# Performance work log

Measured on AMD Instinct MI355X. Metric: run time of the kernel, lower is better.

The kernel has to match this reference:

```python
import jax, jax.numpy as jnp
import numpy as np

HID = 1024
H = 8        # num_attention_heads
KV = 2       # num_key_value_heads
HD = HID // H  # head_dim = 128
G = H // KV    # kv groups = 4
EPS = 1e-6


def setup_inputs() -> dict:
    key = jax.random.key(0)
    ks = jax.random.split(key, 12)
    B, S = 4, 2048
    s = 0.02
    inp = {
        "hidden_states": jax.random.normal(ks[0], (B, S, HID), jnp.float32),
        "rope": jax.random.normal(ks[1], (1, 1, S, 2 * HD), jnp.float32),
        # q_proj outputs 2*H*HD (query + elementwise gate)
        "Wq": jax.random.normal(ks[2], (HID, 2 * H * HD), jnp.float32) * s,
        "bq": jnp.zeros((2 * H * HD,), jnp.float32),
        "Wk": jax.random.normal(ks[3], (HID, KV * HD), jnp.float32) * s,
        "bk": jnp.zeros((KV * HD,), jnp.float32),
        "Wv": jax.random.normal(ks[4], (HID, KV * HD), jnp.float32) * s,
        "bv": jnp.zeros((KV * HD,), jnp.float32),
        "Wo": jax.random.normal(ks[5], (H * HD, HID), jnp.float32) * s,
        "bo": jnp.zeros((HID,), jnp.float32),
        "q_norm_w": jnp.ones((HD,), jnp.float32),
        "k_norm_w": jnp.ones((HD,), jnp.float32),
    }
    return inp


def _rmsnorm(x, w):
    var = jnp.mean(jnp.square(x), axis=-1, keepdims=True)
    return x * jax.lax.rsqrt(var + EPS) * w


def _rot(x):
    # interleaved rotation: [-x1, x0, -x3, x2, ...]
    x2 = x.reshape(x.shape[:-1] + (HD // 2, 2))
    r = jnp.stack([-x2[..., 1], x2[..., 0]], axis=-1)
    return r.reshape(x.shape)


def _apply_rope_cat(x, emb):
    # emb: [S, 2*HD] = cat(sin, cos); x: [B, h, S, HD]
    sin, cos = jnp.split(emb, 2, axis=-1)
    sin = sin[None, None]
    cos = cos[None, None]
    return x * cos + _rot(x) * sin


def reference(hidden_states, rope, Wq, bq, Wk, bk, Wv, bv, Wo, bo, q_norm_w, k_norm_w):
    B, S, _ = hidden_states.shape
    qg = hidden_states @ Wq + bq                     # [B,S,2*H*HD]
    qg = qg.reshape(B, S, KV, -1)                    # [B,S,KV, 2*G*HD]
    q, gate = jnp.split(qg, [HD * G], axis=-1)       # [B,S,KV,G*HD], [B,S,KV,G*HD]
    gate = gate.reshape(B, S, H, HD)                 # [B,S,H,HD]
    q = q.reshape(B, S, H, HD).transpose(0, 2, 1, 3) # [B,H,S,HD]
    k = (hidden_states @ Wk + bk).reshape(B, S, KV, HD).transpose(0, 2, 1, 3)
    v = (hidden_states @ Wv + bv).reshape(B, S, KV, HD).transpose(0, 2, 1, 3)

    q = _rmsnorm(q, q_norm_w)
    k = _rmsnorm(k, k_norm_w)

    emb = rope[0, 0, :S]                             # [S, 2*HD]
    q = _apply_rope_cat(q, emb)
    k = _apply_rope_cat(k, emb)

    # GQA: repeat kv heads to match query heads
    k = jnp.repeat(k, G, axis=1)                     # [B,H,S,HD]
    v = jnp.repeat(v, G, axis=1)

    scale = 1.0 / jnp.sqrt(jnp.asarray(HD, q.dtype))
    scores = jnp.einsum("bhqd,bhkd->bhqk", q, k) * scale
    attn = jax.nn.softmax(scores, axis=-1)
    out = jnp.einsum("bhqk,bhkd->bhqd", attn, v)     # [B,H,S,HD]

    out = out.transpose(0, 2, 1, 3)                  # [B,S,H,HD]
    out = out * jax.nn.sigmoid(gate)
    out = out.reshape(B, S, H * HD)
    return out @ Wo + bo
```

## Files before the change

kernel.cpp:

```cpp
#include <hip/hip_runtime.h>
#include <math.h>

#define SCALE_ 0.08838834764831845f
#define PSHIFT 8.0f

typedef __attribute__((ext_vector_type(8))) short short8;
typedef __attribute__((ext_vector_type(4))) float floatx4;
typedef __attribute__((ext_vector_type(4))) _Float16 half4;

__device__ inline short f2bf(float x) {
    union { float f; unsigned u; } v; v.f = x;
    unsigned r = v.u + 0x7fff + ((v.u >> 16) & 1);
    return (short)(r >> 16);
}
__device__ inline float bf2f(short h) {
    union { float f; unsigned u; } v; v.u = ((unsigned)(unsigned short)h) << 16;
    return v.f;
}

__global__ __launch_bounds__(256) void convert_x(
    const float* __restrict__ X, short* __restrict__ Xb,
    const float* __restrict__ bq, const float* __restrict__ bk2,
    const float* __restrict__ bv2, float* __restrict__ bcat)
{
    const int gid = blockIdx.x * 256 + threadIdx.x;
    if (gid < 2097152) {
        const float4 v = ((const float4*)X)[gid];
        short4 o;
        o.x = f2bf(v.x); o.y = f2bf(v.y); o.z = f2bf(v.z); o.w = f2bf(v.w);
        ((short4*)Xb)[gid] = o;
    }
    if (gid < 2560)
        bcat[gid] = (gid < 2048) ? bq[gid]
                  : (gid < 2304) ? bk2[gid - 2048] : bv2[gid - 2304];
}

__global__ __launch_bounds__(256) void wtrans(
    const float* __restrict__ Wq, const float* __restrict__ Wk,
    const float* __restrict__ Wv, const float* __restrict__ Wo,
    short* __restrict__ Wt, short* __restrict__ Wot)
{
    __shared__ float T[32][33];
    const int t = threadIdx.x;
    const int k0 = blockIdx.x * 32;
    const int ny = blockIdx.y;
    const float* src; int ldn, ncol0, nrow0; short* dst;
    if (ny < 80) {
        const int n0 = ny * 32;
        if (n0 < 2048)      { src = Wq; ldn = 2048; ncol0 = n0; }
        else if (n0 < 2304) { src = Wk; ldn = 256;  ncol0 = n0 - 2048; }
        else                { src = Wv; ldn = 256;  ncol0 = n0 - 2304; }
        dst = Wt; nrow0 = n0;
    } else {
        const int n0 = (ny - 80) * 32;
        src = Wo; ldn = 1024; ncol0 = n0; dst = Wot; nrow0 = n0;
    }
    {
        const int r = t >> 3, c4 = (t & 7) * 4;
        const float4 v = *(const float4*)&src[(size_t)(k0 + r) * ldn + ncol0 + c4];
        T[r][c4 + 0] = v.x; T[r][c4 + 1] = v.y; T[r][c4 + 2] = v.z; T[r][c4 + 3] = v.w;
    }
    __syncthreads();
    {
        const int nr = t >> 3, kc4 = (t & 7) * 4;
        short4 o;
        o.x = f2bf(T[kc4 + 0][nr]);
        o.y = f2bf(T[kc4 + 1][nr]);
        o.z = f2bf(T[kc4 + 2][nr]);
        o.w = f2bf(T[kc4 + 3][nr]);
        *(short4*)&dst[(size_t)(nrow0 + nr) * 1024 + k0 + kc4] = o;
    }
}

__global__ __launch_bounds__(256) void qkv_mfma(
    const short* __restrict__ Ag, const short* __restrict__ Bg,
    const float* __restrict__ bcat,
    short* __restrict__ qb, short* __restrict__ kb,
    short* __restrict__ vb, short* __restrict__ gateb)
{
    __shared__ short As[128 * 64];
    __shared__ short Bs[128 * 64];
    const int tid = threadIdx.x;
    const int wave = tid >> 6, lane = tid & 63;
    const int quad = lane >> 4, l16 = lane & 15;
    const int wm = wave & 1, wn = wave >> 1;
    const int m0 = blockIdx.y * 128, n0 = blockIdx.x * 128;

    floatx4 acc[4][4] = {};

    for (int k0 = 0; k0 < 1024; k0 += 64) {
        __syncthreads();
        #pragma unroll
        for (int c = 0; c < 4; ++c) {
            const int blk = (c * 4 + wave) * 64 + lane;
            const int row = blk >> 3, p = blk & 7;
            const int col = (p ^ (row & 7)) << 3;
            __builtin_amdgcn_global_load_lds(
                (const __attribute__((address_space(1))) unsigned int*)(Ag + (size_t)(m0 + row) * 1024 + k0 + col),
                (__attribute__((address_space(3))) unsigned int*)&As[(c * 4 + wave) * 512],
                16, 0, 0);
            __builtin_amdgcn_global_load_lds(
                (const __attribute__((address_space(1))) unsigned int*)(Bg + (size_t)(n0 + row) * 1024 + k0 + col),
                (__attribute__((address_space(3))) unsigned int*)&Bs[(c * 4 + wave) * 512],
                16, 0, 0);
        }
        __syncthreads();
        #pragma unroll
        for (int ks = 0; ks < 2; ++ks) {
            short8 af[4], bfr[4];
            #pragma unroll
            for (int mt = 0; mt < 4; ++mt) {
                const int row = wm * 64 + mt * 16 + l16;
                const int p = (ks * 4 + quad) ^ (row & 7);
                af[mt] = *(const short8*)&As[row * 64 + p * 8];
            }
            #pragma unroll
            for (int nt = 0; nt < 4; ++nt) {
                const int row = wn * 64 + nt * 16 + l16;
                const int p = (ks * 4 + quad) ^ (row & 7);
                bfr[nt] = *(const short8*)&Bs[row * 64 + p * 8];
            }
            #pragma unroll
            for (int mt = 0; mt < 4; ++mt)
                #pragma unroll
                for (int nt = 0; nt < 4; ++nt)
                    acc[mt][nt] = __builtin_amdgcn_mfma_f32_16x16x32_bf16(af[mt], bfr[nt], acc[mt][nt], 0, 0, 0);
        }
    }

    #pragma unroll
    for (int nt = 0; nt < 4; ++nt) {
        const int n = n0 + wn * 64 + nt * 16 + l16;
        const float bias = bcat[n];
        #pragma unroll
        for (int mt = 0; mt < 4; ++mt) {
            #pragma unroll
            for (int r = 0; r < 4; ++r) {
                const int m = m0 + wm * 64 + mt * 16 + quad * 4 + r;
                const int b = m >> 11, s = m & 2047;
                const short o = f2bf(acc[mt][nt][r] + bias);
                if (n < 2048) {
                    const int kv = n >> 10, rr = n & 1023;
                    if (rr < 512) {
                        const int h = kv * 4 + (rr >> 7), d = rr & 127;
                        qb[(((size_t)(b * 8 + h)) * 2048 + s) * 128 + d] = o;
                    } else {
                        const int r2 = rr - 512;
                        const int h = kv * 4 + (r2 >> 7), d = r2 & 127;
                        gateb[(size_t)m * 1024 + h * 128 + d] = o;
                    }
                } else if (n < 2304) {
                    const int c = n - 2048;
                    kb[(((size_t)(b * 2 + (c >> 7))) * 2048 + s) * 128 + (c & 127)] = o;
                } else {
                    const int c = n - 2304;
                    vb[(((size_t)(b * 2 + (c >> 7))) * 2048 + s) * 128 + (c & 127)] = o;
                }
            }
        }
    }
}

__global__ __launch_bounds__(256) void norm_rope(
    short* __restrict__ qb, short* __restrict__ kb,
    const float* __restrict__ rope,
    const float* __restrict__ qw, const float* __restrict__ kw)
{
    const int row = blockIdx.x * 4 + (threadIdx.x >> 6);
    short* base; const float* w; int s; float scl;
    if (row < 65536) { base = qb + (size_t)row * 128; s = row & 2047; w = qw; scl = SCALE_; }
    else { const int r2 = row - 65536; base = kb + (size_t)r2 * 128; s = r2 & 2047; w = kw; scl = 1.0f; }
    const int lane = threadIdx.x & 63;
    const short2 xv = *(const short2*)&base[lane * 2];
    const float x0 = bf2f(xv.x), x1 = bf2f(xv.y);
    float ssq = x0 * x0 + x1 * x1;
    #pragma unroll
    for (int off = 1; off < 64; off <<= 1) ssq += __shfl_xor(ssq, off);
    const float inv = rsqrtf(ssq * (1.0f / 128.0f) + 1e-6f);
    const float a = x0 * inv * w[lane * 2];
    const float b = x1 * inv * w[lane * 2 + 1];
    const float* er = rope + (size_t)s * 256;
    const float sin0 = er[lane * 2], sin1 = er[lane * 2 + 1];
    const float cos0 = er[128 + lane * 2], cos1 = er[128 + lane * 2 + 1];
    short2 o;
    o.x = f2bf((a * cos0 - b * sin0) * scl);
    o.y = f2bf((b * cos1 + a * sin1) * scl);
    *(short2*)&base[lane * 2] = o;
}

__global__ __launch_bounds__(256) void vtrans(
    const short* __restrict__ vb, _Float16* __restrict__ vt)
{
    __shared__ float T[32][33];
    const int t = threadIdx.x;
    const int s0 = blockIdx.x * 32, d0 = blockIdx.y * 32, bk = blockIdx.z;
    const short* src = vb + ((size_t)bk * 2048 + s0) * 128 + d0;
    {
        const int sr = t >> 3, c4 = (t & 7) * 4;
        const short4 xv = *(const short4*)&src[sr * 128 + c4];
        T[sr][c4 + 0] = bf2f(xv.x);
        T[sr][c4 + 1] = bf2f(xv.y);
        T[sr][c4 + 2] = bf2f(xv.z);
        T[sr][c4 + 3] = bf2f(xv.w);
    }
    __syncthreads();
    {
        const int dr = t >> 3, sc4 = (t & 7) * 4;
        half4 o;
        o[0] = (_Float16)T[sc4 + 0][dr];
        o[1] = (_Float16)T[sc4 + 1][dr];
        o[2] = (_Float16)T[sc4 + 2][dr];
        o[3] = (_Float16)T[sc4 + 3][dr];
        *(half4*)&vt[((size_t)bk * 128 + d0 + dr) * 2048 + s0 + sc4] = o;
    }
}

__global__ __launch_bounds__(256) void attn_mfma(
    const short* __restrict__ qb, const short* __restrict__ kb,
    const _Float16* __restrict__ vt, const short* __restrict__ gateb,
    short* __restrict__ xo)
{
    __shared__ short   Ks[64][132];
    __shared__ _Float16 VTs[128][68];

    const int tid = threadIdx.x;
    const int wave = tid >> 6, lane = tid & 63;
    const int quad = lane >> 4, l16 = lane & 15;
    const int bh = blockIdx.y, b = bh >> 3, h = bh & 7, kv = h >> 2;
    const int q0 = blockIdx.x * 64;

    short8 qf[4];
    {
        const short* qbase = qb + (((size_t)(b * 8 + h)) * 2048 + q0 + wave * 16 + l16) * 128;
        #pragma unroll
        for (int ks = 0; ks < 4; ++ks)
            qf[ks] = *(const short8*)&qbase[ks * 32 + quad * 8];
    }

    const short*    kbase  = kb + (size_t)(b * 2 + kv) * 2048 * 128;
    const _Float16* vtbase = vt + (size_t)(b * 2 + kv) * 128 * 2048;

    floatx4 O[8] = {};
    float lsum = 0.0f;

    for (int kt = 0; kt < 32; ++kt) {
        __syncthreads();
        const short* kg = kbase + (size_t)kt * 64 * 128;
        #pragma unroll
        for (int i = 0; i < 4; ++i) {
            const int idx = tid + i * 256;
            const int r = idx >> 4, c = (idx & 15) * 8;
            *(short8*)&Ks[r][c] = *(const short8*)&kg[r * 128 + c];
        }
        const _Float16* vg = vtbase + kt * 64;
        #pragma unroll
        for (int i = 0; i < 4; ++i) {
            const int idx = tid + i * 256;
            const int r = idx >> 3, c = (idx & 7) * 8;
            *(float4*)&VTs[r][c] = *(const float4*)&vg[(size_t)r * 2048 + c];
        }
        __syncthreads();

        floatx4 ST[4];
        #pragma unroll
        for (int jt = 0; jt < 4; ++jt) {
            ST[jt] = (floatx4){0.f, 0.f, 0.f, 0.f};
            #pragma unroll
            for (int ks = 0; ks < 4; ++ks) {
                const short8 af = *(const short8*)&Ks[jt * 16 + l16][ks * 32 + quad * 8];
                ST[jt] = __builtin_amdgcn_mfma_f32_16x16x32_bf16(af, qf[ks], ST[jt], 0, 0, 0);
            }
        }

        half4 pf[4];
        #pragma unroll
        for (int jt = 0; jt < 4; ++jt) {
            const float p0 = __expf(ST[jt][0] - PSHIFT);
            const float p1 = __expf(ST[jt][1] - PSHIFT);
            const float p2 = __expf(ST[jt][2] - PSHIFT);
            const float p3 = __expf(ST[jt][3] - PSHIFT);
            lsum += (p0 + p1) + (p2 + p3);
            pf[jt][0] = (_Float16)p0;
            pf[jt][1] = (_Float16)p1;
            pf[jt][2] = (_Float16)p2;
            pf[jt][3] = (_Float16)p3;
        }

        #pragma unroll
        for (int jt = 0; jt < 4; ++jt) {
            #pragma unroll
            for (int dt = 0; dt < 8; ++dt) {
                const half4 va = *(const half4*)&VTs[dt * 16 + l16][jt * 16 + quad * 4];
                O[dt] = __builtin_amdgcn_mfma_f32_16x16x16f16(va, pf[jt], O[dt], 0, 0, 0);
            }
        }
    }

    {
        float ps = lsum;
        ps += __shfl_xor(ps, 16);
        ps += __shfl_xor(ps, 32);
        const float invl = 1.0f / ps;
        const int s = q0 + wave * 16 + l16;
        const size_t base = ((size_t)b * 2048 + s) * 1024 + h * 128;
        #pragma unroll
        for (int dt = 0; dt < 8; ++dt) {
            const int d0 = dt * 16 + quad * 4;
            const short4 g4 = *(const short4*)&gateb[base + d0];
            short4 o4;
            o4.x = f2bf(O[dt][0] * invl * (1.0f / (1.0f + __expf(-bf2f(g4.x)))));
            o4.y = f2bf(O[dt][1] * invl * (1.0f / (1.0f + __expf(-bf2f(g4.y)))));
            o4.z = f2bf(O[dt][2] * invl * (1.0f / (1.0f + __expf(-bf2f(g4.z)))));
            o4.w = f2bf(O[dt][3] * invl * (1.0f / (1.0f + __expf(-bf2f(g4.w)))));
            *(short4*)&xo[base + d0] = o4;
        }
    }
}

__global__ __launch_bounds__(256) void out_mfma(
    const short* __restrict__ Ag, const short* __restrict__ Bg,
    const float* __restrict__ bo, float* __restrict__ Y)
{
    __shared__ short As[128 * 64];
    __shared__ short Bs[128 * 64];
    const int tid = threadIdx.x;
    const int wave = tid >> 6, lane = tid & 63;
    const int quad = lane >> 4, l16 = lane & 15;
    const int wm = wave & 1, wn = wave >> 1;
    const int m0 = blockIdx.y * 128, n0 = blockIdx.x * 128;

    floatx4 acc[4][4] = {};

    for (int k0 = 0; k0 < 1024; k0 += 64) {
        __syncthreads();
        #pragma unroll
        for (int c = 0; c < 4; ++c) {
            const int blk = (c * 4 + wave) * 64 + lane;
            const int row = blk >> 3, p = blk & 7;
            const int col = (p ^ (row & 7)) << 3;
            __builtin_amdgcn_global_load_lds(
                (const __attribute__((address_space(1))) unsigned int*)(Ag + (size_t)(m0 + row) * 1024 + k0 + col),
                (__attribute__((address_space(3))) unsigned int*)&As[(c * 4 + wave) * 512],
                16, 0, 0);
            __builtin_amdgcn_global_load_lds(
                (const __attribute__((address_space(1))) unsigned int*)(Bg + (size_t)(n0 + row) * 1024 + k0 + col),
                (__attribute__((address_space(3))) unsigned int*)&Bs[(c * 4 + wave) * 512],
                16, 0, 0);
        }
        __syncthreads();
        #pragma unroll
        for (int ks = 0; ks < 2; ++ks) {
            short8 af[4], bfr[4];
            #pragma unroll
            for (int mt = 0; mt < 4; ++mt) {
                const int row = wm * 64 + mt * 16 + l16;
                const int p = (ks * 4 + quad) ^ (row & 7);
                af[mt] = *(const short8*)&As[row * 64 + p * 8];
            }
            #pragma unroll
            for (int nt = 0; nt < 4; ++nt) {
                const int row = wn * 64 + nt * 16 + l16;
                const int p = (ks * 4 + quad) ^ (row & 7);
                bfr[nt] = *(const short8*)&Bs[row * 64 + p * 8];
            }
            #pragma unroll
            for (int mt = 0; mt < 4; ++mt)
                #pragma unroll
                for (int nt = 0; nt < 4; ++nt)
                    acc[mt][nt] = __builtin_amdgcn_mfma_f32_16x16x32_bf16(af[mt], bfr[nt], acc[mt][nt], 0, 0, 0);
        }
    }

    #pragma unroll
    for (int nt = 0; nt < 4; ++nt) {
        const int n = n0 + wn * 64 + nt * 16 + l16;
        const float bias = bo[n];
        #pragma unroll
        for (int mt = 0; mt < 4; ++mt) {
            #pragma unroll
            for (int r = 0; r < 4; ++r) {
                const int m = m0 + wm * 64 + mt * 16 + quad * 4 + r;
                Y[(size_t)m * 1024 + n] = acc[mt][nt][r] + bias;
            }
        }
    }
}

extern "C" void kernel_launch(void* const* d_in, const int* in_sizes, int n_in,
                              void* d_out, int out_size, void* d_ws, size_t ws_size,
                              hipStream_t stream) {
    (void)in_sizes; (void)n_in; (void)out_size; (void)ws_size;
    const float* hs   = (const float*)d_in[0];
    const float* rope = (const float*)d_in[1];
    const float* Wq   = (const float*)d_in[2];
    const float* bq   = (const float*)d_in[3];
    const float* Wk   = (const float*)d_in[4];
    const float* bk   = (const float*)d_in[5];
    const float* Wv   = (const float*)d_in[6];
    const float* bv   = (const float*)d_in[7];
    const float* Wo   = (const float*)d_in[8];
    const float* bo   = (const float*)d_in[9];
    const float* qw   = (const float*)d_in[10];
    const float* kw   = (const float*)d_in[11];
    float* out = (float*)d_out;

    short* qb    = (short*)d_ws;
    short* kbuf  = qb    + (size_t)8388608;
    short* vb    = kbuf  + (size_t)2097152;
    _Float16* vt = (_Float16*)(vb + (size_t)2097152);
    short* gateb = (short*)(vt + (size_t)2097152);
    short* xb    = gateb + (size_t)8388608;
    short* wt    = xb    + (size_t)8388608;
    short* wot   = wt    + (size_t)2621440;
    float* bcat  = (float*)(wot + (size_t)1048576);

    convert_x<<<dim3(8192), 256, 0, stream>>>(hs, xb, bq, bk, bv, bcat);
    wtrans<<<dim3(32, 112), 256, 0, stream>>>(Wq, Wk, Wv, Wo, wt, wot);
    qkv_mfma<<<dim3(20, 64), 256, 0, stream>>>(xb, wt, bcat, qb, kbuf, vb, gateb);
    norm_rope<<<dim3(20480), 256, 0, stream>>>(qb, kbuf, rope, qw, kw);
    vtrans<<<dim3(64, 4, 8), 256, 0, stream>>>(vb, vt);
    attn_mfma<<<dim3(32, 32), 256, 0, stream>>>(qb, kbuf, vt, gateb, xb);
    out_mfma<<<dim3(8, 64), 256, 0, stream>>>(xb, wot, bo, out);
}
```

Measured before the change: 345.9 us.

## Write V transposed from QKV GEMM and register-prefetch K/V tiles in attention

The QKV GEMM epilogue now writes V straight into the transposed fp16 layout, which removes the separate vtrans kernel along with its extra read and write of V. The attention kernel now loads the next K and V tiles into registers while the current tile is being computed, then stores them to LDS at the start of the following iteration, so global memory latency overlaps with MFMA work. In exchange, the transposed V stores from the epilogue are strided and uncoalesced (2-byte writes with a stride along s), and the register prefetch adds register pressure in the attention kernel.

```diff
diff --git a/kernel.cpp b/kernel.cpp
--- a/kernel.cpp
+++ b/kernel.cpp
@@ -76,7 +76,7 @@
     const short* __restrict__ Ag, const short* __restrict__ Bg,
     const float* __restrict__ bcat,
     short* __restrict__ qb, short* __restrict__ kb,
-    short* __restrict__ vb, short* __restrict__ gateb)
+    _Float16* __restrict__ vt, short* __restrict__ gateb)
 {
     __shared__ short As[128 * 64];
     __shared__ short Bs[128 * 64];
@@ -138,23 +138,24 @@
             for (int r = 0; r < 4; ++r) {
                 const int m = m0 + wm * 64 + mt * 16 + quad * 4 + r;
                 const int b = m >> 11, s = m & 2047;
-                const short o = f2bf(acc[mt][nt][r] + bias);
+                const float val = acc[mt][nt][r] + bias;
                 if (n < 2048) {
                     const int kv = n >> 10, rr = n & 1023;
                     if (rr < 512) {
                         const int h = kv * 4 + (rr >> 7), d = rr & 127;
-                        qb[(((size_t)(b * 8 + h)) * 2048 + s) * 128 + d] = o;
+                        qb[(((size_t)(b * 8 + h)) * 2048 + s) * 128 + d] = f2bf(val);
                     } else {
                         const int r2 = rr - 512;
                         const int h = kv * 4 + (r2 >> 7), d = r2 & 127;
-                        gateb[(size_t)m * 1024 + h * 128 + d] = o;
+                        gateb[(size_t)m * 1024 + h * 128 + d] = f2bf(val);
                     }
                 } else if (n < 2304) {
                     const int c = n - 2048;
-                    kb[(((size_t)(b * 2 + (c >> 7))) * 2048 + s) * 128 + (c & 127)] = o;
+                    kb[(((size_t)(b * 2 + (c >> 7))) * 2048 + s) * 128 + (c & 127)] = f2bf(val);
                 } else {
                     const int c = n - 2304;
-                    vb[(((size_t)(b * 2 + (c >> 7))) * 2048 + s) * 128 + (c & 127)] = o;
+                    const int kvh = c >> 7, d = c & 127;
+                    vt[(((size_t)(b * 2 + kvh)) * 128 + d) * 2048 + s] = (_Float16)val;
                 }
             }
         }
@@ -188,33 +189,6 @@
     *(short2*)&base[lane * 2] = o;
 }
 
-__global__ __launch_bounds__(256) void vtrans(
-    const short* __restrict__ vb, _Float16* __restrict__ vt)
-{
-    __shared__ float T[32][33];
-    const int t = threadIdx.x;
-    const int s0 = blockIdx.x * 32, d0 = blockIdx.y * 32, bk = blockIdx.z;
-    const short* src = vb + ((size_t)bk * 2048 + s0) * 128 + d0;
-    {
-        const int sr = t >> 3, c4 = (t & 7) * 4;
-        const short4 xv = *(const short4*)&src[sr * 128 + c4];
-        T[sr][c4 + 0] = bf2f(xv.x);
-        T[sr][c4 + 1] = bf2f(xv.y);
-        T[sr][c4 + 2] = bf2f(xv.z);
-        T[sr][c4 + 3] = bf2f(xv.w);
-    }
-    __syncthreads();
-    {
-        const int dr = t >> 3, sc4 = (t & 7) * 4;
-        half4 o;
-        o[0] = (_Float16)T[sc4 + 0][dr];
-        o[1] = (_Float16)T[sc4 + 1][dr];
-        o[2] = (_Float16)T[sc4 + 2][dr];
-        o[3] = (_Float16)T[sc4 + 3][dr];
-        *(half4*)&vt[((size_t)bk * 128 + d0 + dr) * 2048 + s0 + sc4] = o;
-    }
-}
-
 __global__ __launch_bounds__(256) void attn_mfma(
     const short* __restrict__ qb, const short* __restrict__ kb,
     const _Float16* __restrict__ vt, const short* __restrict__ gateb,
@@ -240,26 +214,39 @@
     const short*    kbase  = kb + (size_t)(b * 2 + kv) * 2048 * 128;
     const _Float16* vtbase = vt + (size_t)(b * 2 + kv) * 128 * 2048;
 
+    short8 kreg[4];
+    float4 vreg[4];
+    #pragma unroll
+    for (int i = 0; i < 4; ++i) {
+        const int idx = tid + i * 256;
+        kreg[i] = *(const short8*)&kbase[(idx >> 4) * 128 + (idx & 15) * 8];
+        vreg[i] = *(const float4*)&vtbase[(size_t)(idx >> 3) * 2048 + (idx & 7) * 8];
+    }
+
     floatx4 O[8] = {};
     float lsum = 0.0f;
 
     for (int kt = 0; kt < 32; ++kt) {
         __syncthreads();
-        const short* kg = kbase + (size_t)kt * 64 * 128;
         #pragma unroll
         for (int i = 0; i < 4; ++i) {
             const int idx = tid + i * 256;
-            const int r = idx >> 4, c = (idx & 15) * 8;
-            *(short8*)&Ks[r][c] = *(const short8*)&kg[r * 128 + c];
-        }
-        const _Float16* vg = vtbase + kt * 64;
-        #pragma unroll
-        for (int i = 0; i < 4; ++i) {
-            const int idx = tid + i * 256;
-            const int r = idx >> 3, c = (idx & 7) * 8;
-            *(float4*)&VTs[r][c] = *(const float4*)&vg[(size_t)r * 2048 + c];
-        }
-        __syncthreads();
+            *(short8*)&Ks[idx >> 4][(idx & 15) * 8] = kreg[i];
+            *(float4*)&VTs[idx >> 3][(idx & 7) * 8] = vreg[i];
+        }
+        __syncthreads();
+
+        {
+            const int ktn = (kt < 31) ? kt + 1 : 31;
+            const short* kg = kbase + (size_t)ktn * 64 * 128;
+            const _Float16* vg = vtbase + ktn * 64;
+            #pragma unroll
+            for (int i = 0; i < 4; ++i) {
+                const int idx = tid + i * 256;
+                kreg[i] = *(const short8*)&kg[(idx >> 4) * 128 + (idx & 15) * 8];
+                vreg[i] = *(const float4*)&vg[(size_t)(idx >> 3) * 2048 + (idx & 7) * 8];
+            }
+        }
 
         floatx4 ST[4];
         #pragma unroll
@@ -406,8 +393,7 @@
 
     short* qb    = (short*)d_ws;
     short* kbuf  = qb    + (size_t)8388608;
-    short* vb    = kbuf  + (size_t)2097152;
-    _Float16* vt = (_Float16*)(vb + (size_t)2097152);
+    _Float16* vt = (_Float16*)(kbuf + (size_t)2097152);
     short* gateb = (short*)(vt + (size_t)2097152);
     short* xb    = gateb + (size_t)8388608;
     short* wt    = xb    + (size_t)8388608;
@@ -416,9 +402,8 @@
 
     convert_x<<<dim3(8192), 256, 0, stream>>>(hs, xb, bq, bk, bv, bcat);
     wtrans<<<dim3(32, 112), 256, 0, stream>>>(Wq, Wk, Wv, Wo, wt, wot);
-    qkv_mfma<<<dim3(20, 64), 256, 0, stream>>>(xb, wt, bcat, qb, kbuf, vb, gateb);
+    qkv_mfma<<<dim3(20, 64), 256, 0, stream>>>(xb, wt, bcat, qb, kbuf, vt, gateb);
     norm_rope<<<dim3(20480), 256, 0, stream>>>(qb, kbuf, rope, qw, kw);
-    vtrans<<<dim3(64, 4, 8), 256, 0, stream>>>(vb, vt);
     attn_mfma<<<dim3(32, 32), 256, 0, stream>>>(qb, kbuf, vt, gateb, xb);
     out_mfma<<<dim3(8, 64), 256, 0, stream>>>(xb, wot, bo, out);
 }
```

New measurement: 397.9 us. 15.0% more time.
